# Performance work log

Measured on AMD Instinct MI355X. Metric: run time of the kernel, lower is better.

The kernel has to match this reference:

```python
import jax, jax.numpy as jnp
import numpy as np

N_NODES = 100000
N_EDGES = 3200000
IN_DIM = 128
HID = 64
N_GRAPHS = 64
BN_EPS = 1e-5


def setup_inputs() -> dict:
    key = jax.random.key(0)
    ks = jax.random.split(key, 12)
    x = jax.random.normal(ks[0], (N_NODES, IN_DIM), dtype=jnp.float32)
    edge_index = jax.random.randint(ks[1], (2, N_EDGES), 0, N_NODES, dtype=jnp.int64)
    edge_weight = jax.random.uniform(ks[2], (N_EDGES,), dtype=jnp.float32)
    batch = jnp.sort(jax.random.randint(ks[3], (N_NODES,), 0, N_GRAPHS, dtype=jnp.int64))
    s1 = 1.0 / np.sqrt(IN_DIM)
    s2 = 1.0 / np.sqrt(HID)
    W1 = jax.random.uniform(ks[4], (IN_DIM, HID), jnp.float32, -s1, s1)
    b1 = jnp.zeros((HID,), jnp.float32)
    W2 = jax.random.uniform(ks[5], (HID, HID), jnp.float32, -s2, s2)
    b2 = jnp.zeros((HID,), jnp.float32)
    g1 = jnp.ones((HID,), jnp.float32)
    be1 = jnp.zeros((HID,), jnp.float32)
    g2 = jnp.ones((HID,), jnp.float32)
    be2 = jnp.zeros((HID,), jnp.float32)
    Wout = jax.random.uniform(ks[6], (HID, 1), jnp.float32, -s2, s2)
    bout = jnp.zeros((1,), jnp.float32)
    return {"x": x, "edge_index": edge_index, "edge_weight": edge_weight,
            "batch": batch, "W1": W1, "b1": b1, "W2": W2, "b2": b2,
            "g1": g1, "be1": be1, "g2": g2, "be2": be2,
            "Wout": Wout, "bout": bout}


def _gcn_norm(edge_index, edge_weight, n_nodes):
    """Add self-loops and compute symmetric GCN normalization coefficients."""
    loop = jnp.arange(n_nodes, dtype=edge_index.dtype)
    row = jnp.concatenate([edge_index[0], loop])   # source nodes
    col = jnp.concatenate([edge_index[1], loop])   # target nodes
    w = jnp.concatenate([edge_weight, jnp.ones((n_nodes,), edge_weight.dtype)])
    deg = jax.ops.segment_sum(w, col, num_segments=n_nodes)
    dinv = jnp.where(deg > 0, jax.lax.rsqrt(jnp.where(deg > 0, deg, 1.0)), 0.0)
    norm = dinv[row] * w * dinv[col]
    return row, col, norm


def _gcn_layer(h, row, col, norm, W, b, n_nodes):
    h = h @ W                                             # [N, H]
    msg = h[row] * norm[:, None]                          # gather + scale
    agg = jax.ops.segment_sum(msg, col, num_segments=n_nodes)  # scatter-add
    return agg + b


def _batchnorm(h, gamma, beta):
    mean = jnp.mean(h, axis=0)
    var = jnp.mean(jnp.square(h - mean), axis=0)
    return gamma * (h - mean) * jax.lax.rsqrt(var + BN_EPS) + beta


def reference(x, edge_index, edge_weight, batch, W1, b1, W2, b2,
              g1, be1, g2, be2, Wout, bout):
    n = x.shape[0]
    row, col, norm = _gcn_norm(edge_index, edge_weight, n)
    # layer 1: GCNConv -> BN -> ReLU (dropout = identity in eval)
    h = _gcn_layer(x, row, col, norm, W1, b1, n)
    h = jax.nn.relu(_batchnorm(h, g1, be1))
    # layer 2
    h = _gcn_layer(h, row, col, norm, W2, b2, n)
    h = jax.nn.relu(_batchnorm(h, g2, be2))
    # global mean pool over graphs
    sums = jax.ops.segment_sum(h, batch, num_segments=N_GRAPHS)
    counts = jax.ops.segment_sum(jnp.ones((n,), h.dtype), batch, num_segments=N_GRAPHS)
    pooled = sums / jnp.maximum(counts, 1.0)[:, None]
    return pooled @ Wout + bout
```

## Files before the change

### kernel.cpp

```cpp
#include <hip/hip_runtime.h>
#include <stdint.h>

#define N_NODES 100000
#define N_EDGES 3200000
#define IN_DIM 128
#define HID 64
#define N_GRAPHS 64
#define BN_EPS 1e-5f
#define NSHARD 16
#define BUCK_SH 7
#define BUCK_SZ 128
#define NBUCK ((N_NODES + BUCK_SZ - 1) / BUCK_SZ)
#define NCNT (NBUCK * 8)
#define BINB_EDGES 4096
#define BIN_BLOCKS ((N_EDGES + BINB_EDGES - 1) / BINB_EDGES)
#define SLOT_CAP 768
#define BCAP 4608
#define SORT_CAP (8 * SLOT_CAP)
#define AGG_CAP 2048

typedef float vf4 __attribute__((ext_vector_type(4)));
typedef int   vi4 __attribute__((ext_vector_type(4)));
typedef unsigned vu2 __attribute__((ext_vector_type(2)));
typedef _Float16 vh4 __attribute__((ext_vector_type(4)));

__device__ __forceinline__ float4 nt_f4(const float* p) {
    vf4 v = __builtin_nontemporal_load((const vf4*)p);
    return make_float4(v.x, v.y, v.z, v.w);
}
__device__ __forceinline__ int4 nt_i4(const int* p) {
    vi4 v = __builtin_nontemporal_load((const vi4*)p);
    return make_int4(v.x, v.y, v.z, v.w);
}
__device__ __forceinline__ uint2 nt_u2(const uint2* p) {
    vu2 v = __builtin_nontemporal_load((const vu2*)p);
    return make_uint2(v.x, v.y);
}
__device__ __forceinline__ unsigned nt_u(const unsigned* p) {
    return __builtin_nontemporal_load(p);
}
__device__ __forceinline__ vh4 nt_h4(const _Float16* p) {
    return __builtin_nontemporal_load((const vh4*)p);
}

__device__ __forceinline__ unsigned pack_edge(unsigned r, _Float16 w) {
    unsigned short hb = __builtin_bit_cast(unsigned short, w);
    return (r << 15) | (unsigned)hb;
}
__device__ __forceinline__ float unpack_w(unsigned u) {
    return (float)__builtin_bit_cast(_Float16, (unsigned short)(u & 0x7FFFu));
}
__device__ __forceinline__ float f16lo(unsigned u) {
    return (float)__builtin_bit_cast(_Float16, (unsigned short)(u & 0xFFFFu));
}
__device__ __forceinline__ float f16hi(unsigned u) {
    return (float)__builtin_bit_cast(_Float16, (unsigned short)(u >> 16));
}
__device__ __forceinline__ unsigned packh2(float a, float b) {
    unsigned short la = __builtin_bit_cast(unsigned short, (_Float16)a);
    unsigned short lb = __builtin_bit_cast(unsigned short, (_Float16)b);
    return (unsigned)la | ((unsigned)lb << 16);
}

__global__ void k_init(int* __restrict__ cur) {
    int i = blockIdx.x * blockDim.x + threadIdx.x;
    if (i < NCNT) cur[i] = i * SLOT_CAP;
}

__global__ __launch_bounds__(512) void k_bin(const int* __restrict__ ei,
                                             const float* __restrict__ ew,
                                             int* __restrict__ cur,
                                             uint2* __restrict__ ebuf) {
    __shared__ int hist[NBUCK];
    int b = blockIdx.x, t = threadIdx.x;
    int s = b & 7;
    int base = b * BINB_EDGES;
    int n = min(BINB_EDGES, N_EDGES - base);
    for (int i = t; i < NBUCK; i += 512) hist[i] = 0;
    __syncthreads();
#pragma unroll
    for (int k = 0; k < 2; ++k) {
        int ch = t + 512 * k;
        if (4 * ch < n) {
            int4 c4 = nt_i4(ei + N_EDGES + base + 4 * ch);
            atomicAdd(&hist[c4.x >> BUCK_SH], 1);
            atomicAdd(&hist[c4.y >> BUCK_SH], 1);
            atomicAdd(&hist[c4.z >> BUCK_SH], 1);
            atomicAdd(&hist[c4.w >> BUCK_SH], 1);
        }
    }
    __syncthreads();
    for (int j = t; j < NBUCK; j += 512) {
        int h = hist[j];
        if (h > 0) hist[j] = atomicAdd(&cur[s * NBUCK + j], h);
    }
    __syncthreads();
#pragma unroll
    for (int k = 0; k < 2; ++k) {
        int ch = t + 512 * k;
        if (4 * ch < n) {
            int4 r4 = nt_i4(ei + base + 4 * ch);
            int4 c4 = nt_i4(ei + N_EDGES + base + 4 * ch);
            float4 w4 = nt_f4(ew + base + 4 * ch);
            int rr[4] = {r4.x, r4.y, r4.z, r4.w};
            int cc[4] = {c4.x, c4.y, c4.z, c4.w};
            float ww[4] = {w4.x, w4.y, w4.z, w4.w};
            int pos[4];
#pragma unroll
            for (int u = 0; u < 4; ++u)
                pos[u] = atomicAdd(&hist[cc[u] >> BUCK_SH], 1);
#pragma unroll
            for (int u = 0; u < 4; ++u)
                ebuf[pos[u]] = make_uint2(
                    (unsigned)(rr[u] | ((cc[u] & (BUCK_SZ - 1)) << 17)),
                    __float_as_uint(ww[u]));
        }
    }
}

__global__ __launch_bounds__(512) void k_sortnorm(const uint2* __restrict__ ebuf,
                                                  const int* __restrict__ cur,
                                                  float* __restrict__ dinv,
                                                  unsigned* __restrict__ ebuf2,
                                                  int2* __restrict__ nrange) {
    __shared__ unsigned sex[SORT_CAP];
    __shared__ _Float16 sew[SORT_CAP];
    __shared__ float sdi[BUCK_SZ];
    __shared__ int scnt[BUCK_SZ];
    __shared__ int scur[BUCK_SZ];
    __shared__ int slen[8], soffc[8];
    int b = blockIdx.x, t = threadIdx.x;
    if (t < BUCK_SZ) { sdi[t] = 0.f; scnt[t] = 0; }
    if (t < 8) slen[t] = cur[t * NBUCK + b] - (t * NBUCK + b) * SLOT_CAP;
    __syncthreads();
    if (t == 0) {
        int run = 0;
#pragma unroll
        for (int s = 0; s < 8; ++s) { soffc[s] = run; run += slen[s]; }
    }
    __syncthreads();
    for (int s = 0; s < 8; ++s) {
        int sb = (s * NBUCK + b) * SLOT_CAP;
        int len = slen[s];
        int off = soffc[s];
        for (int i = t; i < len; i += 512) {
            uint2 u = nt_u2(ebuf + sb + i);
            float wf = __uint_as_float(u.y);
            sex[off + i] = u.x;
            sew[off + i] = (_Float16)wf;
            int cl = u.x >> 17;
            atomicAdd(&sdi[cl], wf);
            atomicAdd(&scnt[cl], 1);
        }
    }
    __syncthreads();
    int n = soffc[7] + slen[7];
    if (t < BUCK_SZ) {
        float di = rsqrtf(sdi[t] + 1.0f);
        int node = b * BUCK_SZ + t;
        if (node < N_NODES) dinv[node] = di;
    }
    __syncthreads();
    for (int off = 1; off < BUCK_SZ; off <<= 1) {
        int x = 0;
        if (t < BUCK_SZ && t >= off) x = scnt[t - off];
        __syncthreads();
        if (t < BUCK_SZ) scnt[t] += x;
        __syncthreads();
    }
    if (t < BUCK_SZ) {
        int excl = (t > 0) ? scnt[t - 1] : 0;
        int cnt = scnt[t] - excl;
        scur[t] = b * BCAP + excl;
        int node = b * BUCK_SZ + t;
        if (node < N_NODES) nrange[node] = make_int2(b * BCAP + excl, b * BCAP + excl + cnt);
    }
    __syncthreads();
    for (int i = t; i < n; i += 512) {
        unsigned x = sex[i];
        unsigned r = x & 131071u;
        int cl = x >> 17;
        int p = atomicAdd(&scur[cl], 1);
        ebuf2[p] = pack_edge(r, sew[i]);
    }
}

template <int K, bool BNH>
__global__ __launch_bounds__(256) void k_gemm(const void* __restrict__ in_,
                                              const float* __restrict__ W,
                                              const float* __restrict__ scale,
                                              const float* __restrict__ shift,
                                              const float* __restrict__ dinv,
                                              _Float16* __restrict__ out) {
    __shared__ float ws[K * 64];
    __shared__ float xs[32 * 132];
    __shared__ float ssc[64], ssh[64];
    int t = threadIdx.x;
    int nbase = blockIdx.x * 128;

#pragma unroll
    for (int i = 0; i < K / 16; ++i) {
        int idx = t + 256 * i;
        ((float4*)ws)[idx] = ((const float4*)W)[idx];
    }
    if (BNH && t < 64) { ssc[t] = scale[t]; ssh[t] = shift[t]; }

    int cg = t & 15;
    int ng = t >> 4;
    float acc[8][4];
#pragma unroll
    for (int i = 0; i < 8; ++i)
#pragma unroll
        for (int j = 0; j < 4; ++j) acc[i][j] = 0.f;

    for (int k0 = 0; k0 < K; k0 += 32) {
        __syncthreads();
#pragma unroll
        for (int i = 0; i < 4; ++i) {
            int idx = t + 256 * i;
            int row = idx >> 3;
            int kq = idx & 7;
            int node = nbase + row;
            float vv[4] = {0.f, 0.f, 0.f, 0.f};
            if (node < N_NODES) {
                if (BNH) {
                    vh4 v = nt_h4((const _Float16*)in_ + (size_t)node * K + k0 + kq * 4);
                    vv[0] = (float)v.x; vv[1] = (float)v.y;
                    vv[2] = (float)v.z; vv[3] = (float)v.w;
                } else {
                    float4 v = nt_f4((const float*)in_ + (size_t)node * K + k0 + kq * 4);
                    vv[0] = v.x; vv[1] = v.y; vv[2] = v.z; vv[3] = v.w;
                }
            }
#pragma unroll
            for (int u = 0; u < 4; ++u) {
                float val = vv[u];
                if (BNH) {
                    int k = k0 + kq * 4 + u;
                    val = fmaxf(ssc[k] * val + ssh[k], 0.f);
                }
                xs[(kq * 4 + u) * 132 + row] = val;
            }
        }
        __syncthreads();
#pragma unroll
        for (int k = 0; k < 32; ++k) {
            float4 wv = *(const float4*)(ws + (k0 + k) * 64 + cg * 4);
            float4 xa = *(const float4*)(xs + k * 132 + ng * 8);
            float4 xb = *(const float4*)(xs + k * 132 + ng * 8 + 4);
            float xv[8] = {xa.x, xa.y, xa.z, xa.w, xb.x, xb.y, xb.z, xb.w};
            float wvv[4] = {wv.x, wv.y, wv.z, wv.w};
#pragma unroll
            for (int i = 0; i < 8; ++i)
#pragma unroll
                for (int j = 0; j < 4; ++j) acc[i][j] += xv[i] * wvv[j];
        }
    }
#pragma unroll
    for (int i = 0; i < 8; ++i) {
        int node = nbase + ng * 8 + i;
        if (node < N_NODES) {
            float dv = dinv[node];
            vh4 o;
            o.x = (_Float16)(acc[i][0] * dv); o.y = (_Float16)(acc[i][1] * dv);
            o.z = (_Float16)(acc[i][2] * dv); o.w = (_Float16)(acc[i][3] * dv);
            *(vh4*)(out + (size_t)node * 64 + cg * 4) = o;
        }
    }
}

__global__ __launch_bounds__(256) void k_agg(const _Float16* __restrict__ hin,
                                             const unsigned* __restrict__ ebuf2,
                                             const int2* __restrict__ nrange,
                                             const float* __restrict__ dinv,
                                             const float* __restrict__ bias,
                                             _Float16* __restrict__ hout,
                                             float* __restrict__ bn_shard) {
    __shared__ unsigned sme[AGG_CAP];
    __shared__ float sm[4][64], qm[4][64];
    int b = blockIdx.x, t = threadIdx.x;
    int wave = t >> 6, lane = t & 63;
    int half = lane >> 5, hl = lane & 31;
    const unsigned* hinu = (const unsigned*)hin;
    int vbase0 = b * 32;
    int ebeg = nrange[vbase0].x;
    int eend = nrange[vbase0 + 31].y;
    int n = eend - ebeg;
    bool fit = (n <= AGG_CAP);
    if (fit) {
        for (int i = t; i < n; i += 256) sme[i] = nt_u(ebuf2 + ebeg + i);
    }
    __syncthreads();

    float s0 = 0.f, q0 = 0.f, s1 = 0.f, q1 = 0.f;
    float bl0 = bias[2 * hl], bl1 = bias[2 * hl + 1];
    int vbase = vbase0 + wave * 8;
    for (int vi = 0; vi < 8; ++vi) {
        int v = vbase + vi;
        int2 be = nrange[v];
        int end = be.y;
        float a0 = 0.f, a1 = 0.f;
        int j = be.x + half;
        if (fit) {
            int jl = j - ebeg;
            for (; j + 16 <= end; j += 16, jl += 16) {
                float fw[8];
                unsigned hv[8];
#pragma unroll
                for (int u = 0; u < 8; ++u) {
                    unsigned e = sme[jl + 2 * u];
                    fw[u] = unpack_w(e);
                    hv[u] = hinu[((size_t)(e >> 15) << 5) + hl];
                }
#pragma unroll
                for (int u = 0; u < 8; ++u) {
                    a0 = fmaf(fw[u], f16lo(hv[u]), a0);
                    a1 = fmaf(fw[u], f16hi(hv[u]), a1);
                }
            }
            for (; j < end; j += 2, jl += 2) {
                unsigned e = sme[jl];
                float fw = unpack_w(e);
                unsigned hv = hinu[((size_t)(e >> 15) << 5) + hl];
                a0 = fmaf(fw, f16lo(hv), a0);
                a1 = fmaf(fw, f16hi(hv), a1);
            }
        } else {
            for (; j + 16 <= end; j += 16) {
                float fw[8];
                unsigned hv[8];
#pragma unroll
                for (int u = 0; u < 8; ++u) {
                    unsigned e = nt_u(ebuf2 + j + 2 * u);
                    fw[u] = unpack_w(e);
                    hv[u] = hinu[((size_t)(e >> 15) << 5) + hl];
                }
#pragma unroll
                for (int u = 0; u < 8; ++u) {
                    a0 = fmaf(fw[u], f16lo(hv[u]), a0);
                    a1 = fmaf(fw[u], f16hi(hv[u]), a1);
                }
            }
            for (; j < end; j += 2) {
                unsigned e = nt_u(ebuf2 + j);
                float fw = unpack_w(e);
                unsigned hv = hinu[((size_t)(e >> 15) << 5) + hl];
                a0 = fmaf(fw, f16lo(hv), a0);
                a1 = fmaf(fw, f16hi(hv), a1);
            }
        }
        a0 += __shfl_xor(a0, 32);
        a1 += __shfl_xor(a1, 32);
        unsigned hv = hinu[((size_t)v << 5) + hl];
        float dv = dinv[v];
        a0 = fmaf(dv, a0 + f16lo(hv), bl0);
        a1 = fmaf(dv, a1 + f16hi(hv), bl1);
        if (half == 0) {
            ((unsigned*)hout)[((size_t)v << 5) + hl] = packh2(a0, a1);
            s0 += a0; q0 += a0 * a0;
            s1 += a1; q1 += a1 * a1;
        }
    }
    if (half == 0) {
        sm[wave][2 * hl] = s0; sm[wave][2 * hl + 1] = s1;
        qm[wave][2 * hl] = q0; qm[wave][2 * hl + 1] = q1;
    }
    __syncthreads();
    if (wave == 0) {
        float ts = sm[0][lane] + sm[1][lane] + sm[2][lane] + sm[3][lane];
        float tq = qm[0][lane] + qm[1][lane] + qm[2][lane] + qm[3][lane];
        float* shard = bn_shard + (blockIdx.x & (NSHARD - 1)) * 128;
        atomicAdd(&shard[lane], ts);
        atomicAdd(&shard[64 + lane], tq);
    }
}

__global__ void k_bn_final(float* __restrict__ bn_shard, const float* __restrict__ gamma,
                           const float* __restrict__ beta, float* __restrict__ scale,
                           float* __restrict__ shift) {
    int t = threadIdx.x;
    if (t < 64) {
        float s = 0.f, q = 0.f;
        for (int i = 0; i < NSHARD; ++i) {
            s += bn_shard[i * 128 + t];
            q += bn_shard[i * 128 + 64 + t];
        }
        float mean = s * (1.0f / N_NODES);
        float var = q * (1.0f / N_NODES) - mean * mean;
        float sc = gamma[t] * rsqrtf(var + BN_EPS);
        scale[t] = sc;
        shift[t] = beta[t] - mean * sc;
    }
    __syncthreads();
    for (int i = t; i < NSHARD * 128; i += 256) bn_shard[i] = 0.f;
}

__global__ __launch_bounds__(256) void k_pool(const _Float16* __restrict__ a2,
                                              const float* __restrict__ scale,
                                              const float* __restrict__ shift,
                                              const int* __restrict__ batch,
                                              float* __restrict__ pooled_sh,
                                              float* __restrict__ pcnt_sh) {
    int b = blockIdx.x, t = threadIdx.x;
    int c = t & 63;
    int rg = t >> 6;
    int base = b * BUCK_SZ;
    float sc = scale[c], sh = shift[c];
    float* pool_s = pooled_sh + (size_t)(b & (NSHARD - 1)) * (N_GRAPHS * 64);
    float* pcnt_s = pcnt_sh + (size_t)(b & (NSHARD - 1)) * N_GRAPHS;
    int gcur = -1;
    float acc = 0.f, cacc = 0.f;
    for (int i = rg; i < BUCK_SZ; i += 4) {
        int v = base + i;
        if (v >= N_NODES) break;
        int g = batch[v];
        if (g != gcur) {
            if (gcur >= 0) {
                atomicAdd(&pool_s[gcur * 64 + c], acc);
                if (c == 0) atomicAdd(&pcnt_s[gcur], cacc);
            }
            gcur = g;
            acc = 0.f;
            cacc = 0.f;
        }
        float h = fmaxf(sc * (float)a2[(size_t)v * 64 + c] + sh, 0.f);
        acc += h;
        cacc += 1.f;
    }
    if (gcur >= 0) {
        atomicAdd(&pool_s[gcur * 64 + c], acc);
        if (c == 0) atomicAdd(&pcnt_s[gcur], cacc);
    }
}

__global__ void k_out(const float* __restrict__ pooled_sh,
                      const float* __restrict__ pcnt_sh,
                      const float* __restrict__ Wout, const float* __restrict__ bout,
                      float* __restrict__ out) {
    int g = threadIdx.x;
    if (g < N_GRAPHS) {
        float cnt = 0.f;
        for (int s = 0; s < NSHARD; ++s) cnt += pcnt_sh[s * N_GRAPHS + g];
        cnt = fmaxf(cnt, 1.0f);
        float sum = 0.f;
        for (int c = 0; c < 64; ++c) {
            float p = 0.f;
            for (int s = 0; s < NSHARD; ++s)
                p += pooled_sh[(size_t)s * N_GRAPHS * 64 + g * 64 + c];
            sum += p * Wout[c];
        }
        out[g] = sum / cnt + bout[0];
    }
}

extern "C" void kernel_launch(void* const* d_in, const int* in_sizes, int n_in,
                              void* d_out, int out_size, void* d_ws, size_t ws_size,
                              hipStream_t stream) {
    const float* x    = (const float*)d_in[0];
    const int*   ei   = (const int*)d_in[1];
    const float* ew   = (const float*)d_in[2];
    const int*   batch= (const int*)d_in[3];
    const float* W1   = (const float*)d_in[4];
    const float* b1   = (const float*)d_in[5];
    const float* W2   = (const float*)d_in[6];
    const float* b2   = (const float*)d_in[7];
    const float* g1   = (const float*)d_in[8];
    const float* be1  = (const float*)d_in[9];
    const float* g2   = (const float*)d_in[10];
    const float* be2  = (const float*)d_in[11];
    const float* Wout = (const float*)d_in[12];
    const float* bout = (const float*)d_in[13];
    float* out = (float*)d_out;

    char* w = (char*)d_ws;
    size_t o = 0;
    auto alloc = [&](size_t bytes) -> void* {
        void* p = w + o;
        o = (o + bytes + 255) & ~(size_t)255;
        return p;
    };
    int*   cur     = (int*)alloc(NCNT * 4);
    int2*  nrange  = (int2*)alloc((size_t)N_NODES * 8);
    float* dinv    = (float*)alloc(N_NODES * 4);
    float* bnshard = (float*)alloc(NSHARD * 128 * 4);
    float* scale1  = (float*)alloc(64 * 4);
    float* shift1  = (float*)alloc(64 * 4);
    float* scale2  = (float*)alloc(64 * 4);
    float* shift2  = (float*)alloc(64 * 4);
    float* pooled  = (float*)alloc(NSHARD * N_GRAPHS * 64 * 4);
    float* pcnt    = (float*)alloc(NSHARD * N_GRAPHS * 4);
    unsigned* ebuf2 = (unsigned*)alloc((size_t)NBUCK * BCAP * 4);
    uint2* ebuf    = (uint2*)alloc((size_t)NCNT * SLOT_CAP * 8);
    _Float16* bufHA = (_Float16*)ebuf;
    _Float16* bufHB = bufHA + (size_t)N_NODES * 64;
    if (o > ws_size) return;

    (void)hipMemsetAsync(bnshard, 0, NSHARD * 128 * 4, stream);
    (void)hipMemsetAsync(pooled, 0, NSHARD * N_GRAPHS * 64 * 4, stream);
    (void)hipMemsetAsync(pcnt, 0, NSHARD * N_GRAPHS * 4, stream);

    k_init<<<(NCNT + 255) / 256, 256, 0, stream>>>(cur);
    k_bin<<<BIN_BLOCKS, 512, 0, stream>>>(ei, ew, cur, ebuf);
    k_sortnorm<<<NBUCK, 512, 0, stream>>>(ebuf, cur, dinv, ebuf2, nrange);

    k_gemm<128, false><<<(N_NODES + 127) / 128, 256, 0, stream>>>(x, W1, nullptr, nullptr, dinv, bufHA);
    k_agg<<<N_NODES / 32, 256, 0, stream>>>(bufHA, ebuf2, nrange, dinv, b1, bufHB, bnshard);
    k_bn_final<<<1, 256, 0, stream>>>(bnshard, g1, be1, scale1, shift1);

    k_gemm<64, true><<<(N_NODES + 127) / 128, 256, 0, stream>>>(bufHB, W2, scale1, shift1, dinv, bufHA);
    k_agg<<<N_NODES / 32, 256, 0, stream>>>(bufHA, ebuf2, nrange, dinv, b2, bufHB, bnshard);
    k_bn_final<<<1, 256, 0, stream>>>(bnshard, g2, be2, scale2, shift2);

    k_pool<<<NBUCK, 256, 0, stream>>>(bufHB, scale2, shift2, batch, pooled, pcnt);
    k_out<<<1, 64, 0, stream>>>(pooled, pcnt, Wout, bout, out);
}
```

Before: 349.3 us.

## Use fp16 MFMA 16x16x32 instructions for the node feature GEMM

Replaces the scalar FP32 register-tiled GEMM in k_gemm with MFMA fp16 matrix instructions. Weights are converted to fp16 and repacked into an MFMA operand layout in shared memory, and activation tiles are stored as fp16 with a padded row stride. The aim is to cut the ALU cost of the feature transform. The costs are that inputs are rounded to fp16 before the multiply, output stores become scalar 2-byte writes, and the weight repack runs per block with strided global reads.

```diff
diff --git a/kernel.cpp b/kernel.cpp
--- a/kernel.cpp
+++ b/kernel.cpp
@@ -23,6 +23,7 @@
 typedef int   vi4 __attribute__((ext_vector_type(4)));
 typedef unsigned vu2 __attribute__((ext_vector_type(2)));
 typedef _Float16 vh4 __attribute__((ext_vector_type(4)));
+typedef _Float16 vh8 __attribute__((ext_vector_type(8)));
 
 __device__ __forceinline__ float4 nt_f4(const float* p) {
     vf4 v = __builtin_nontemporal_load((const vf4*)p);
@@ -192,79 +193,82 @@
                                               const float* __restrict__ shift,
                                               const float* __restrict__ dinv,
                                               _Float16* __restrict__ out) {
-    __shared__ float ws[K * 64];
-    __shared__ float xs[32 * 132];
+    constexpr int KT = K / 32;
+    __shared__ vh8 sW[KT * 4 * 64];
+    __shared__ _Float16 sA[128 * 40];
     __shared__ float ssc[64], ssh[64];
     int t = threadIdx.x;
+    int lane = t & 63, wave = t >> 6;
     int nbase = blockIdx.x * 128;
-
-#pragma unroll
-    for (int i = 0; i < K / 16; ++i) {
-        int idx = t + 256 * i;
-        ((float4*)ws)[idx] = ((const float4*)W)[idx];
-    }
     if (BNH && t < 64) { ssc[t] = scale[t]; ssh[t] = shift[t]; }
 
-    int cg = t & 15;
-    int ng = t >> 4;
-    float acc[8][4];
-#pragma unroll
-    for (int i = 0; i < 8; ++i)
-#pragma unroll
-        for (int j = 0; j < 4; ++j) acc[i][j] = 0.f;
-
-    for (int k0 = 0; k0 < K; k0 += 32) {
+    for (int eidx = t; eidx < KT * 4 * 64; eidx += 256) {
+        int l = eidx & 63, ct = (eidx >> 6) & 3, kt = eidx >> 8;
+        int kb = kt * 32 + (l >> 4) * 8;
+        int col = ct * 16 + (l & 15);
+        vh8 h;
+#pragma unroll
+        for (int e = 0; e < 8; ++e) h[e] = (_Float16)W[(kb + e) * 64 + col];
+        sW[eidx] = h;
+    }
+
+    vf4 acc[2][4];
+#pragma unroll
+    for (int i = 0; i < 2; ++i)
+#pragma unroll
+        for (int j = 0; j < 4; ++j) acc[i][j] = (vf4){0.f, 0.f, 0.f, 0.f};
+
+    for (int kt = 0; kt < KT; ++kt) {
         __syncthreads();
 #pragma unroll
         for (int i = 0; i < 4; ++i) {
             int idx = t + 256 * i;
-            int row = idx >> 3;
-            int kq = idx & 7;
+            int row = idx >> 3, kq = idx & 7;
             int node = nbase + row;
             float vv[4] = {0.f, 0.f, 0.f, 0.f};
             if (node < N_NODES) {
                 if (BNH) {
-                    vh4 v = nt_h4((const _Float16*)in_ + (size_t)node * K + k0 + kq * 4);
+                    vh4 v = nt_h4((const _Float16*)in_ + (size_t)node * K + kt * 32 + kq * 4);
                     vv[0] = (float)v.x; vv[1] = (float)v.y;
                     vv[2] = (float)v.z; vv[3] = (float)v.w;
+#pragma unroll
+                    for (int u = 0; u < 4; ++u) {
+                        int k = kt * 32 + kq * 4 + u;
+                        vv[u] = fmaxf(ssc[k] * vv[u] + ssh[k], 0.f);
+                    }
                 } else {
-                    float4 v = nt_f4((const float*)in_ + (size_t)node * K + k0 + kq * 4);
+                    float4 v = nt_f4((const float*)in_ + (size_t)node * K + kt * 32 + kq * 4);
                     vv[0] = v.x; vv[1] = v.y; vv[2] = v.z; vv[3] = v.w;
                 }
             }
-#pragma unroll
-            for (int u = 0; u < 4; ++u) {
-                float val = vv[u];
-                if (BNH) {
-                    int k = k0 + kq * 4 + u;
-                    val = fmaxf(ssc[k] * val + ssh[k], 0.f);
-                }
-                xs[(kq * 4 + u) * 132 + row] = val;
-            }
+            vh4 hv;
+            hv.x = (_Float16)vv[0]; hv.y = (_Float16)vv[1];
+            hv.z = (_Float16)vv[2]; hv.w = (_Float16)vv[3];
+            *(vh4*)(sA + row * 40 + kq * 4) = hv;
         }
         __syncthreads();
-#pragma unroll
-        for (int k = 0; k < 32; ++k) {
-            float4 wv = *(const float4*)(ws + (k0 + k) * 64 + cg * 4);
-            float4 xa = *(const float4*)(xs + k * 132 + ng * 8);
-            float4 xb = *(const float4*)(xs + k * 132 + ng * 8 + 4);
-            float xv[8] = {xa.x, xa.y, xa.z, xa.w, xb.x, xb.y, xb.z, xb.w};
-            float wvv[4] = {wv.x, wv.y, wv.z, wv.w};
-#pragma unroll
-            for (int i = 0; i < 8; ++i)
-#pragma unroll
-                for (int j = 0; j < 4; ++j) acc[i][j] += xv[i] * wvv[j];
-        }
-    }
-#pragma unroll
-    for (int i = 0; i < 8; ++i) {
-        int node = nbase + ng * 8 + i;
-        if (node < N_NODES) {
-            float dv = dinv[node];
-            vh4 o;
-            o.x = (_Float16)(acc[i][0] * dv); o.y = (_Float16)(acc[i][1] * dv);
-            o.z = (_Float16)(acc[i][2] * dv); o.w = (_Float16)(acc[i][3] * dv);
-            *(vh4*)(out + (size_t)node * 64 + cg * 4) = o;
+        vh8 a0 = *(const vh8*)(sA + (wave * 32 + (lane & 15)) * 40 + (lane >> 4) * 8);
+        vh8 a1 = *(const vh8*)(sA + (wave * 32 + 16 + (lane & 15)) * 40 + (lane >> 4) * 8);
+#pragma unroll
+        for (int ct = 0; ct < 4; ++ct) {
+            vh8 bfr = sW[(kt * 4 + ct) * 64 + lane];
+            acc[0][ct] = __builtin_amdgcn_mfma_f32_16x16x32_f16(a0, bfr, acc[0][ct], 0, 0, 0);
+            acc[1][ct] = __builtin_amdgcn_mfma_f32_16x16x32_f16(a1, bfr, acc[1][ct], 0, 0, 0);
+        }
+    }
+    int colb = lane & 15, rq = lane >> 4;
+#pragma unroll
+    for (int rti = 0; rti < 2; ++rti) {
+#pragma unroll
+        for (int r = 0; r < 4; ++r) {
+            int node = nbase + wave * 32 + rti * 16 + rq * 4 + r;
+            if (node < N_NODES) {
+                float dv = dinv[node];
+#pragma unroll
+                for (int ct = 0; ct < 4; ++ct)
+                    out[(size_t)node * 64 + ct * 16 + colb] =
+                        (_Float16)(acc[rti][ct][r] * dv);
+            }
         }
     }
 }
```

Result: faster. 310.6 us (-11.1%).
